# Kernel tuning notes

Measured on AMD Instinct MI355X. Metric: run time of the kernel, lower is better.

## Reference

```python
import jax, jax.numpy as jnp
import numpy as np


def _pairwise_sq_dists(t):
    # t: [B, L, R] -> [B, L, L] squared L2 distances via ||a||^2+||b||^2-2a.b
    sq = jnp.sum(t * t, axis=-1)                      # [B, L]
    dots = jnp.einsum('bir,bjr->bij', t, t)           # [B, L, L]
    d = sq[:, :, None] + sq[:, None, :] - 2.0 * dots
    return jnp.maximum(d, 0.0)


def setup_inputs() -> dict:
    key = jax.random.key(0)
    k1, k2, k3 = jax.random.split(key, 3)
    B, L, D, H, R = 16, 1024, 1024, 1024, 128
    batch = jax.random.normal(k1, (B, L, D), dtype=jnp.float32)
    # Linear weights stored as [in, out]; small init to keep activations sane
    W1 = jax.random.normal(k2, (D, H), dtype=jnp.float32) * (1.0 / np.sqrt(D))
    b1 = jnp.zeros((H,), dtype=jnp.float32)
    W2 = jax.random.normal(k3, (H, R), dtype=jnp.float32) * (1.0 / np.sqrt(H))
    b2 = jnp.zeros((R,), dtype=jnp.float32)
    return {"batch": batch, "W1": W1, "b1": b1, "W2": W2, "b2": b2}


def reference(batch, W1, b1, W2, b2):
    # layer 1: Linear + clamp(min=0)
    h = jnp.maximum(jnp.einsum('bld,dh->blh', batch, W1) + b1, 0.0)
    # layer 2 (projection to probe rank): Linear + clamp(min=0)
    t = jnp.maximum(jnp.einsum('blh,hr->blr', h, W2) + b2, 0.0)
    # all-pairs squared distances per sentence: [B, L, L]
    return _pairwise_sq_dists(t)
```

## Files before the change

### kernel.cpp

```cpp
#include <hip/hip_runtime.h>
#include <stdint.h>

#define B_ 16
#define L_ 1024
#define D_ 1024
#define H_ 1024
#define R_ 128
#define M_ (B_ * L_)

using f32x4  = __attribute__((ext_vector_type(4))) float;
using bf16x8 = __attribute__((ext_vector_type(8))) short;

__device__ __forceinline__ short f2bf(float f) {
  uint32_t u = __builtin_bit_cast(uint32_t, f);
  u = (u + 0x7FFFu + ((u >> 16) & 1u)) >> 16;
  return (short)(uint16_t)u;
}
__device__ __forceinline__ float bf2f(uint16_t h) {
  return __builtin_bit_cast(float, (uint32_t)h << 16);
}

__global__ void k_f32_to_bf16(const float* __restrict__ in, short* __restrict__ out) {
  size_t i = ((size_t)blockIdx.x * blockDim.x + threadIdx.x) * 8;
  float4 a = *(const float4*)(in + i);
  float4 b = *(const float4*)(in + i + 4);
  union { short s[8]; bf16x8 v; } o;
  o.s[0] = f2bf(a.x); o.s[1] = f2bf(a.y); o.s[2] = f2bf(a.z); o.s[3] = f2bf(a.w);
  o.s[4] = f2bf(b.x); o.s[5] = f2bf(b.y); o.s[6] = f2bf(b.z); o.s[7] = f2bf(b.w);
  *(bf16x8*)(out + i) = o.v;
}

__global__ void k_transpose_bf16(const float* __restrict__ in, short* __restrict__ out,
                                 int K, int N) {
  __shared__ float s[64][65];
  int n0 = blockIdx.x * 64, k0 = blockIdx.y * 64;
  int tx = threadIdx.x & 63, tq = threadIdx.x >> 6;
#pragma unroll
  for (int j = 0; j < 16; ++j) {
    int r = j * 4 + tq;
    s[r][tx] = in[(size_t)(k0 + r) * N + (n0 + tx)];
  }
  __syncthreads();
#pragma unroll
  for (int j = 0; j < 16; ++j) {
    int r = j * 4 + tq;
    out[(size_t)(n0 + r) * K + (k0 + tx)] = f2bf(s[tx][r]);
  }
}

__global__ __launch_bounds__(256)
void k_gemm_bias_relu(const short* __restrict__ A, const short* __restrict__ Bt,
                      const float* __restrict__ bias, short* __restrict__ C,
                      int M, int N, int K) {
  __shared__ __align__(16) short As[128 * 32];
  __shared__ __align__(16) short Bs[128 * 32];
  const int tid = threadIdx.x, lane = tid & 63, wave = tid >> 6;
  const int wr = wave >> 1, wc = wave & 1;
  const int m0 = blockIdx.y * 128, n0 = blockIdx.x * 128;
  const int lrow = lane & 15, lk8 = (lane >> 4) * 8;
  const int srow = lane >> 2;
  const int skc  = (lane & 3) * 8;

  f32x4 acc[4][4] = {};

  for (int k0 = 0; k0 < K; k0 += 32) {
#pragma unroll
    for (int c = 0; c < 2; ++c) {
      int chunk = wave * 2 + c;
      int row = chunk * 16 + srow;
      const short* ga = A  + (size_t)(m0 + row) * K + (k0 + skc);
      const short* gb = Bt + (size_t)(n0 + row) * K + (k0 + skc);
      __builtin_amdgcn_global_load_lds(
          (const __attribute__((address_space(1))) void*)ga,
          (__attribute__((address_space(3))) void*)(As + chunk * 512 + lane * 8), 16, 0, 0);
      __builtin_amdgcn_global_load_lds(
          (const __attribute__((address_space(1))) void*)gb,
          (__attribute__((address_space(3))) void*)(Bs + chunk * 512 + lane * 8), 16, 0, 0);
    }
    __syncthreads();

    bf16x8 af[4], bfr[4];
#pragma unroll
    for (int m = 0; m < 4; ++m)
      af[m] = *(const bf16x8*)(As + (wr * 64 + m * 16 + lrow) * 32 + lk8);
#pragma unroll
    for (int n = 0; n < 4; ++n)
      bfr[n] = *(const bf16x8*)(Bs + (wc * 64 + n * 16 + lrow) * 32 + lk8);
#pragma unroll
    for (int m = 0; m < 4; ++m)
#pragma unroll
      for (int n = 0; n < 4; ++n)
        acc[m][n] = __builtin_amdgcn_mfma_f32_16x16x32_bf16(af[m], bfr[n], acc[m][n], 0, 0, 0);
    __syncthreads();
  }

  const int rbase = m0 + wr * 64 + (lane >> 4) * 4;
  const int cbase = n0 + wc * 64 + lrow;
#pragma unroll
  for (int n = 0; n < 4; ++n) {
    const int col = cbase + n * 16;
    const float bn = bias[col];
#pragma unroll
    for (int m = 0; m < 4; ++m) {
      const int row = rbase + m * 16;
#pragma unroll
      for (int r = 0; r < 4; ++r) {
        float v = acc[m][n][r] + bn;
        C[(size_t)(row + r) * N + col] = f2bf(fmaxf(v, 0.f));
      }
    }
  }
}

__global__ void k_rowsq(const short* __restrict__ T, float* __restrict__ sq) {
  int row  = blockIdx.x * 4 + (threadIdx.x >> 6);
  int lane = threadIdx.x & 63;
  uint32_t u = *(const uint32_t*)(T + (size_t)row * R_ + lane * 2);
  float a = bf2f((uint16_t)(u & 0xffffu));
  float b = bf2f((uint16_t)(u >> 16));
  float s = a * a + b * b;
#pragma unroll
  for (int o = 32; o >= 1; o >>= 1) s += __shfl_xor(s, o, 64);
  if (lane == 0) sq[row] = s;
}

__global__ __launch_bounds__(256)
void k_pairwise(const short* __restrict__ T, const float* __restrict__ sq,
                float* __restrict__ out) {
  __shared__ __align__(16) short As[128 * 32];
  __shared__ __align__(16) short Bs[128 * 32];
  const int b = blockIdx.z;
  const short* Tb  = T  + (size_t)b * L_ * R_;
  const float* sqb = sq + (size_t)b * L_;
  const int tid = threadIdx.x, lane = tid & 63, wave = tid >> 6;
  const int wr = wave >> 1, wc = wave & 1;
  const int m0 = blockIdx.y * 128, n0 = blockIdx.x * 128;
  const int lrow = lane & 15, lk8 = (lane >> 4) * 8;
  const int srow = lane >> 2;
  const int skc  = (lane & 3) * 8;

  f32x4 acc[4][4] = {};

  for (int k0 = 0; k0 < R_; k0 += 32) {
#pragma unroll
    for (int c = 0; c < 2; ++c) {
      int chunk = wave * 2 + c;
      int row = chunk * 16 + srow;
      const short* ga = Tb + (size_t)(m0 + row) * R_ + (k0 + skc);
      const short* gb = Tb + (size_t)(n0 + row) * R_ + (k0 + skc);
      __builtin_amdgcn_global_load_lds(
          (const __attribute__((address_space(1))) void*)ga,
          (__attribute__((address_space(3))) void*)(As + chunk * 512 + lane * 8), 16, 0, 0);
      __builtin_amdgcn_global_load_lds(
          (const __attribute__((address_space(1))) void*)gb,
          (__attribute__((address_space(3))) void*)(Bs + chunk * 512 + lane * 8), 16, 0, 0);
    }
    __syncthreads();

    bf16x8 af[4], bfr[4];
#pragma unroll
    for (int m = 0; m < 4; ++m)
      af[m] = *(const bf16x8*)(As + (wr * 64 + m * 16 + lrow) * 32 + lk8);
#pragma unroll
    for (int n = 0; n < 4; ++n)
      bfr[n] = *(const bf16x8*)(Bs + (wc * 64 + n * 16 + lrow) * 32 + lk8);
#pragma unroll
    for (int m = 0; m < 4; ++m)
#pragma unroll
      for (int n = 0; n < 4; ++n)
        acc[m][n] = __builtin_amdgcn_mfma_f32_16x16x32_bf16(af[m], bfr[n], acc[m][n], 0, 0, 0);
    __syncthreads();
  }

  const int rbase = m0 + wr * 64 + (lane >> 4) * 4;
  const int cbase = n0 + wc * 64 + lrow;
  float sqj[4];
#pragma unroll
  for (int n = 0; n < 4; ++n) sqj[n] = sqb[cbase + n * 16];
#pragma unroll
  for (int m = 0; m < 4; ++m) {
#pragma unroll
    for (int r = 0; r < 4; ++r) {
      const int row = rbase + m * 16 + r;
      const float sqi = sqb[row];
      float* orow = out + ((size_t)b * L_ + row) * L_;
#pragma unroll
      for (int n = 0; n < 4; ++n) {
        float d = sqi + sqj[n] - 2.0f * acc[m][n][r];
        orow[cbase + n * 16] = fmaxf(d, 0.f);
      }
    }
  }
}

extern "C" void kernel_launch(void* const* d_in, const int* in_sizes, int n_in,
                              void* d_out, int out_size, void* d_ws, size_t ws_size,
                              hipStream_t stream) {
  const float* X  = (const float*)d_in[0];
  const float* W1 = (const float*)d_in[1];
  const float* b1 = (const float*)d_in[2];
  const float* W2 = (const float*)d_in[3];
  const float* b2 = (const float*)d_in[4];
  float* out = (float*)d_out;

  char* ws = (char*)d_ws;
  size_t off = 0;
  auto alloc = [&](size_t bytes) {
    char* p = ws + off;
    off += (bytes + 255) & ~(size_t)255;
    return p;
  };
  short* Xb  = (short*)alloc((size_t)M_ * D_ * 2);
  short* W1t = (short*)alloc((size_t)H_ * D_ * 2);
  short* Hb  = (short*)alloc((size_t)M_ * H_ * 2);
  short* W2t = (short*)alloc((size_t)R_ * H_ * 2);
  short* Tb  = (short*)alloc((size_t)M_ * R_ * 2);
  float* Sq  = (float*)alloc((size_t)M_ * 4);

  k_f32_to_bf16<<<((size_t)M_ * D_) / 2048, 256, 0, stream>>>(X, Xb);
  k_transpose_bf16<<<dim3(H_ / 64, D_ / 64), 256, 0, stream>>>(W1, W1t, D_, H_);
  k_transpose_bf16<<<dim3(R_ / 64, H_ / 64), 256, 0, stream>>>(W2, W2t, H_, R_);
  k_gemm_bias_relu<<<dim3(H_ / 128, M_ / 128), 256, 0, stream>>>(Xb, W1t, b1, Hb, M_, H_, D_);
  k_gemm_bias_relu<<<dim3(R_ / 128, M_ / 128), 256, 0, stream>>>(Hb, W2t, b2, Tb, M_, R_, H_);
  k_rowsq<<<M_ / 4, 256, 0, stream>>>(Tb, Sq);
  k_pairwise<<<dim3(L_ / 128, L_ / 128, B_), 256, 0, stream>>>(Tb, Sq, out);
}
```

Baseline: 228.8 us.

## Split-K the second GEMM, fuse bias/relu/rowsq into reduce, swizzle GEMM1 blocks for XCD locality

```diff
diff --git a/kernel.cpp b/kernel.cpp
--- a/kernel.cpp
+++ b/kernel.cpp
@@ -48,28 +48,25 @@
   }
 }
 
-__global__ __launch_bounds__(256)
-void k_gemm_bias_relu(const short* __restrict__ A, const short* __restrict__ Bt,
-                      const float* __restrict__ bias, short* __restrict__ C,
-                      int M, int N, int K) {
-  __shared__ __align__(16) short As[128 * 32];
-  __shared__ __align__(16) short Bs[128 * 32];
+__device__ __forceinline__ void gemm_body_128(const short* __restrict__ Ap,
+                                              const short* __restrict__ Bp,
+                                              int ld, int kSteps,
+                                              short* As, short* Bs,
+                                              f32x4 (&acc)[4][4]) {
   const int tid = threadIdx.x, lane = tid & 63, wave = tid >> 6;
   const int wr = wave >> 1, wc = wave & 1;
-  const int m0 = blockIdx.y * 128, n0 = blockIdx.x * 128;
   const int lrow = lane & 15, lk8 = (lane >> 4) * 8;
   const int srow = lane >> 2;
   const int skc  = (lane & 3) * 8;
 
-  f32x4 acc[4][4] = {};
-
-  for (int k0 = 0; k0 < K; k0 += 32) {
+  for (int ks = 0; ks < kSteps; ++ks) {
+    const int k0 = ks * 32;
 #pragma unroll
     for (int c = 0; c < 2; ++c) {
       int chunk = wave * 2 + c;
       int row = chunk * 16 + srow;
-      const short* ga = A  + (size_t)(m0 + row) * K + (k0 + skc);
-      const short* gb = Bt + (size_t)(n0 + row) * K + (k0 + skc);
+      const short* ga = Ap + (size_t)row * ld + (k0 + skc);
+      const short* gb = Bp + (size_t)row * ld + (k0 + skc);
       __builtin_amdgcn_global_load_lds(
           (const __attribute__((address_space(1))) void*)ga,
           (__attribute__((address_space(3))) void*)(As + chunk * 512 + lane * 8), 16, 0, 0);
@@ -93,9 +90,27 @@
         acc[m][n] = __builtin_amdgcn_mfma_f32_16x16x32_bf16(af[m], bfr[n], acc[m][n], 0, 0, 0);
     __syncthreads();
   }
-
+}
+
+__global__ __launch_bounds__(256)
+void k_gemm1(const short* __restrict__ A, const short* __restrict__ Bt,
+             const float* __restrict__ bias, short* __restrict__ C) {
+  __shared__ __align__(16) short As[128 * 32];
+  __shared__ __align__(16) short Bs[128 * 32];
+  const int b = blockIdx.x;
+  const int xcd = b & 7, seq = b >> 3;
+  const int g = xcd + ((seq >> 6) << 3);
+  const int i = seq & 63;
+  const int m0 = (g * 8 + (i >> 3)) * 128;
+  const int n0 = (i & 7) * 128;
+
+  f32x4 acc[4][4] = {};
+  gemm_body_128(A + (size_t)m0 * D_, Bt + (size_t)n0 * D_, D_, D_ / 32, As, Bs, acc);
+
+  const int lane = threadIdx.x & 63, wave = threadIdx.x >> 6;
+  const int wr = wave >> 1, wc = wave & 1;
   const int rbase = m0 + wr * 64 + (lane >> 4) * 4;
-  const int cbase = n0 + wc * 64 + lrow;
+  const int cbase = n0 + wc * 64 + (lane & 15);
 #pragma unroll
   for (int n = 0; n < 4; ++n) {
     const int col = cbase + n * 16;
@@ -106,22 +121,57 @@
 #pragma unroll
       for (int r = 0; r < 4; ++r) {
         float v = acc[m][n][r] + bn;
-        C[(size_t)(row + r) * N + col] = f2bf(fmaxf(v, 0.f));
+        C[(size_t)(row + r) * H_ + col] = f2bf(fmaxf(v, 0.f));
       }
     }
   }
 }
 
-__global__ void k_rowsq(const short* __restrict__ T, float* __restrict__ sq) {
-  int row  = blockIdx.x * 4 + (threadIdx.x >> 6);
-  int lane = threadIdx.x & 63;
-  uint32_t u = *(const uint32_t*)(T + (size_t)row * R_ + lane * 2);
-  float a = bf2f((uint16_t)(u & 0xffffu));
-  float b = bf2f((uint16_t)(u >> 16));
-  float s = a * a + b * b;
-#pragma unroll
-  for (int o = 32; o >= 1; o >>= 1) s += __shfl_xor(s, o, 64);
-  if (lane == 0) sq[row] = s;
+__global__ __launch_bounds__(256)
+void k_gemm2_splitk(const short* __restrict__ A, const short* __restrict__ Bt,
+                    float* __restrict__ P) {
+  __shared__ __align__(16) short As[128 * 32];
+  __shared__ __align__(16) short Bs[128 * 32];
+  const int m0 = blockIdx.y * 128;
+  const int s  = blockIdx.z;
+  const int kOff = s * (H_ / 4);
+
+  f32x4 acc[4][4] = {};
+  gemm_body_128(A + (size_t)m0 * H_ + kOff, Bt + kOff, H_, (H_ / 4) / 32, As, Bs, acc);
+
+  const int lane = threadIdx.x & 63, wave = threadIdx.x >> 6;
+  const int wr = wave >> 1, wc = wave & 1;
+  const int rbase = wr * 64 + (lane >> 4) * 4;
+  const int cbase = wc * 64 + (lane & 15);
+  float* Ps = P + (size_t)s * M_ * R_ + (size_t)m0 * R_;
+#pragma unroll
+  for (int m = 0; m < 4; ++m)
+#pragma unroll
+    for (int r = 0; r < 4; ++r)
+#pragma unroll
+      for (int n = 0; n < 4; ++n)
+        Ps[(size_t)(rbase + m * 16 + r) * R_ + cbase + n * 16] = acc[m][n][r];
+}
+
+__global__ void k_reduce2(const float* __restrict__ P, const float* __restrict__ b2,
+                          short* __restrict__ T, float* __restrict__ sq) {
+  const int row  = blockIdx.x * 4 + (threadIdx.x >> 6);
+  const int lane = threadIdx.x & 63;
+  const int c0 = lane * 2;
+  float s0 = 0.f, s1 = 0.f;
+#pragma unroll
+  for (int s = 0; s < 4; ++s) {
+    const float2 v = *(const float2*)(P + ((size_t)s * M_ + row) * R_ + c0);
+    s0 += v.x; s1 += v.y;
+  }
+  float v0 = fmaxf(s0 + b2[c0], 0.f);
+  float v1 = fmaxf(s1 + b2[c0 + 1], 0.f);
+  uint32_t pk = (uint32_t)(uint16_t)f2bf(v0) | ((uint32_t)(uint16_t)f2bf(v1) << 16);
+  *(uint32_t*)(T + (size_t)row * R_ + c0) = pk;
+  float q = v0 * v0 + v1 * v1;
+#pragma unroll
+  for (int o = 32; o >= 1; o >>= 1) q += __shfl_xor(q, o, 64);
+  if (lane == 0) sq[row] = q;
 }
 
 __global__ __launch_bounds__(256)
@@ -132,48 +182,15 @@
   const int b = blockIdx.z;
   const short* Tb  = T  + (size_t)b * L_ * R_;
   const float* sqb = sq + (size_t)b * L_;
-  const int tid = threadIdx.x, lane = tid & 63, wave = tid >> 6;
-  const int wr = wave >> 1, wc = wave & 1;
   const int m0 = blockIdx.y * 128, n0 = blockIdx.x * 128;
-  const int lrow = lane & 15, lk8 = (lane >> 4) * 8;
-  const int srow = lane >> 2;
-  const int skc  = (lane & 3) * 8;
 
   f32x4 acc[4][4] = {};
-
-  for (int k0 = 0; k0 < R_; k0 += 32) {
-#pragma unroll
-    for (int c = 0; c < 2; ++c) {
-      int chunk = wave * 2 + c;
-      int row = chunk * 16 + srow;
-      const short* ga = Tb + (size_t)(m0 + row) * R_ + (k0 + skc);
-      const short* gb = Tb + (size_t)(n0 + row) * R_ + (k0 + skc);
-      __builtin_amdgcn_global_load_lds(
-          (const __attribute__((address_space(1))) void*)ga,
-          (__attribute__((address_space(3))) void*)(As + chunk * 512 + lane * 8), 16, 0, 0);
-      __builtin_amdgcn_global_load_lds(
-          (const __attribute__((address_space(1))) void*)gb,
-          (__attribute__((address_space(3))) void*)(Bs + chunk * 512 + lane * 8), 16, 0, 0);
-    }
-    __syncthreads();
-
-    bf16x8 af[4], bfr[4];
-#pragma unroll
-    for (int m = 0; m < 4; ++m)
-      af[m] = *(const bf16x8*)(As + (wr * 64 + m * 16 + lrow) * 32 + lk8);
-#pragma unroll
-    for (int n = 0; n < 4; ++n)
-      bfr[n] = *(const bf16x8*)(Bs + (wc * 64 + n * 16 + lrow) * 32 + lk8);
-#pragma unroll
-    for (int m = 0; m < 4; ++m)
-#pragma unroll
-      for (int n = 0; n < 4; ++n)
-        acc[m][n] = __builtin_amdgcn_mfma_f32_16x16x32_bf16(af[m], bfr[n], acc[m][n], 0, 0, 0);
-    __syncthreads();
-  }
-
+  gemm_body_128(Tb + (size_t)m0 * R_, Tb + (size_t)n0 * R_, R_, R_ / 32, As, Bs, acc);
+
+  const int lane = threadIdx.x & 63, wave = threadIdx.x >> 6;
+  const int wr = wave >> 1, wc = wave & 1;
   const int rbase = m0 + wr * 64 + (lane >> 4) * 4;
-  const int cbase = n0 + wc * 64 + lrow;
+  const int cbase = n0 + wc * 64 + (lane & 15);
   float sqj[4];
 #pragma unroll
   for (int n = 0; n < 4; ++n) sqj[n] = sqb[cbase + n * 16];
@@ -216,12 +233,13 @@
   short* W2t = (short*)alloc((size_t)R_ * H_ * 2);
   short* Tb  = (short*)alloc((size_t)M_ * R_ * 2);
   float* Sq  = (float*)alloc((size_t)M_ * 4);
+  float* P   = (float*)Xb;
 
   k_f32_to_bf16<<<((size_t)M_ * D_) / 2048, 256, 0, stream>>>(X, Xb);
   k_transpose_bf16<<<dim3(H_ / 64, D_ / 64), 256, 0, stream>>>(W1, W1t, D_, H_);
   k_transpose_bf16<<<dim3(R_ / 64, H_ / 64), 256, 0, stream>>>(W2, W2t, H_, R_);
-  k_gemm_bias_relu<<<dim3(H_ / 128, M_ / 128), 256, 0, stream>>>(Xb, W1t, b1, Hb, M_, H_, D_);
-  k_gemm_bias_relu<<<dim3(R_ / 128, M_ / 128), 256, 0, stream>>>(Hb, W2t, b2, Tb, M_, R_, H_);
-  k_rowsq<<<M_ / 4, 256, 0, stream>>>(Tb, Sq);
+  k_gemm1<<<dim3((M_ / 128) * (H_ / 128)), 256, 0, stream>>>(Xb, W1t, b1, Hb);
+  k_gemm2_splitk<<<dim3(1, M_ / 128, 4), 256, 0, stream>>>(Hb, W2t, P);
+  k_reduce2<<<M_ / 4, 256, 0, stream>>>(P, b2, Tb, Sq);
   k_pairwise<<<dim3(L_ / 128, L_ / 128, B_), 256, 0, stream>>>(Tb, Sq, out);
 }
```

New measurement: 209.6 us. -8.4%, faster.
